# Kernel optimization log

Hardware: AMD Instinct MI355X
Metric: run time of the kernel (lower is better)

## Reference

```python
import jax, jax.numpy as jnp
import numpy as np
import math

B, L, DIM = 128, 192, 512
NTOKEN = 100
MAX_BONDS = 6
MAX_LEN = 192


def _sinusoidal_pe(max_len, dim):
    pos = np.arange(max_len, dtype=np.float32)[:, None]
    div = np.exp(np.arange(0, dim, 2, dtype=np.float32) * (-math.log(10000.0) / dim))
    pe = np.zeros((max_len, dim), dtype=np.float32)
    pe[:, 0::2] = np.sin(pos * div)
    pe[:, 1::2] = np.cos(pos * div)
    return jnp.asarray(pe[:, None, :])  # [max_len, 1, dim]


def setup_inputs() -> dict:
    key = jax.random.key(0)
    ks = jax.random.split(key, 16)
    s = 0.02
    inp = {
        "element": jax.random.randint(ks[0], (B, L), 0, NTOKEN),
        "bond": jax.random.randint(ks[1], (B, L, MAX_BONDS), 0, L),
        "aroma": jax.random.randint(ks[2], (B, L), 0, 2),
        "charge": jax.random.randint(ks[3], (B, L), 0, 6),
        "segment": jax.random.randint(ks[4], (B, L), 0, 30),
        # parameters
        "pe": _sinusoidal_pe(MAX_LEN, DIM),
        "E_elem": jax.random.normal(ks[5], (NTOKEN, DIM), jnp.float32) * s,
        "E_charge": jax.random.normal(ks[6], (13, DIM), jnp.float32) * s,
        "E_aroma": jax.random.normal(ks[7], (2, DIM), jnp.float32) * s,
        "E_seg": jax.random.normal(ks[8], (30, DIM), jnp.float32) * s,
        "W1": jax.random.normal(ks[9], (DIM, 4 * DIM), jnp.float32) * s,
        "b1": jnp.zeros((4 * DIM,), jnp.float32),
        "W2": jax.random.normal(ks[10], (4 * DIM, DIM), jnp.float32) * s,
        "b2": jnp.zeros((DIM,), jnp.float32),
        "W3": jax.random.normal(ks[11], (DIM, 4 * DIM), jnp.float32) * s,
        "b3": jnp.zeros((4 * DIM,), jnp.float32),
        "W4": jax.random.normal(ks[12], (4 * DIM, DIM), jnp.float32) * s,
        "b4": jnp.zeros((DIM,), jnp.float32),
        "W5": jax.random.normal(ks[13], (DIM, DIM), jnp.float32) * s,
        "b5": jnp.zeros((DIM,), jnp.float32),
    }
    return inp


def _mlp(x, W1, b1, W2, b2, W3, b3, W4, b4, W5, b5):
    x = x + jnp.maximum(x @ W1 + b1, 0.0) @ W2 + b2
    x = x + jnp.maximum(x @ W3 + b3, 0.0) @ W4 + b4
    return x @ W5 + b5


def reference(element, bond, aroma, charge, segment, pe,
              E_elem, E_charge, E_aroma, E_seg,
              W1, b1, W2, b2, W3, b3, W4, b4, W5, b5):
    b, l = element.shape
    # embeddings: all [l, b, dim]
    emb = E_elem[element.T]
    emb = emb + pe[:l]                      # [l,1,dim] broadcast (eval: dropout off)
    emb = emb + E_aroma[aroma.T]
    emb = emb + E_charge[charge.T + 6]
    emb = emb + E_seg[segment.T]
    message = _mlp(emb, W1, b1, W2, b2, W3, b3, W4, b4, W5, b5)  # [l,b,dim]
    # bond aggregation: agg[k] = sum_m message[bond[b,k,m]] excluding self-bonds
    # (equivalent to the dense one-hot einsum with the diagonal masked out)
    msg_bld = jnp.transpose(message, (1, 0, 2))          # [b,l,dim]
    g = msg_bld[jnp.arange(b)[:, None, None], bond]      # [b,l,MAX_BONDS,dim]
    mask = (bond != jnp.arange(l)[None, :, None]).astype(message.dtype)
    agg = jnp.einsum('bkmd,bkm->bkd', g, mask)           # [b,l,dim]
    return emb + jnp.transpose(agg, (1, 0, 2))           # [l,b,dim]
```

## Files before the change

### kernel.cpp

```cpp
#include <hip/hip_runtime.h>
#include <cstdint>
#include <cstddef>

typedef unsigned short u16;
typedef unsigned int u32;

typedef unsigned short u16x8 __attribute__((ext_vector_type(8)));
typedef __bf16 bf16x8 __attribute__((ext_vector_type(8)));
typedef float f32x4 __attribute__((ext_vector_type(4)));
typedef float f32x8 __attribute__((ext_vector_type(8)));

#define NB   128
#define NL   192
#define NTOK (NB * NL)
#define DIM  512
#define HID  2048

static __device__ __forceinline__ float bf2f(u16 h) {
    union { u32 u; float f; } v; v.u = ((u32)h) << 16; return v.f;
}
static __device__ __forceinline__ u16 f2bf(float f) {
    union { float f; u32 u; } v; v.f = f;
    u32 u = v.u + 0x7FFF + ((v.u >> 16) & 1);
    return (u16)(u >> 16);
}

__global__ void transpose_f2b(const float* __restrict__ in, u16* __restrict__ out,
                              int K, int N) {
    __shared__ float tile[32][33];
    int tx = threadIdx.x & 31, ty = threadIdx.x >> 5;
    int n0 = blockIdx.x * 32, k0 = blockIdx.y * 32;
#pragma unroll
    for (int i = 0; i < 4; i++)
        tile[ty + i * 8][tx] = in[(size_t)(k0 + ty + i * 8) * N + n0 + tx];
    __syncthreads();
#pragma unroll
    for (int i = 0; i < 4; i++)
        out[(size_t)(n0 + ty + i * 8) * K + k0 + tx] = f2bf(tile[tx][ty + i * 8]);
}

static __device__ __forceinline__ void add8f(float* acc, const float* p) {
    f32x8 v = *(const f32x8*)p;
#pragma unroll
    for (int i = 0; i < 8; i++) acc[i] += v[i];
}

__global__ void embed_kernel(const int* __restrict__ element, const int* __restrict__ aroma,
                             const int* __restrict__ charge, const int* __restrict__ segment,
                             const float* __restrict__ pe, const float* __restrict__ E_elem,
                             const float* __restrict__ E_charge, const float* __restrict__ E_aroma,
                             const float* __restrict__ E_seg,
                             float* __restrict__ emb32, u16* __restrict__ emb16) {
    int t = blockIdx.x * 4 + (threadIdx.x >> 6);
    int lane = threadIdx.x & 63;
    int l = t >> 7, b = t & 127;
    int d = lane * 8;
    int idx = b * NL + l;
    int e = element[idx];
    int a = aroma[idx];
    int c = charge[idx] + 6;
    int s = segment[idx];
    float acc[8] = {0, 0, 0, 0, 0, 0, 0, 0};
    add8f(acc, E_elem  + (size_t)e * DIM + d);
    add8f(acc, pe      + (size_t)l * DIM + d);
    add8f(acc, E_aroma + (size_t)a * DIM + d);
    add8f(acc, E_charge+ (size_t)c * DIM + d);
    add8f(acc, E_seg   + (size_t)s * DIM + d);
    f32x8 o32; u16x8 o16;
#pragma unroll
    for (int i = 0; i < 8; i++) { o32[i] = acc[i]; o16[i] = f2bf(acc[i]); }
    *(f32x8*)(emb32 + (size_t)t * DIM + d) = o32;
    *(u16x8*)(emb16 + (size_t)t * DIM + d) = o16;
}

__global__ __launch_bounds__(256, 2) void gemm_bt(
    const u16* __restrict__ A, const u16* __restrict__ BT,
    const float* __restrict__ bias, const u16* __restrict__ resid16,
    const float* __restrict__ resid32,
    u16* __restrict__ C, int M, int N, int K, int do_relu) {
    __shared__ __align__(16) u16 smem[3 * 128 * 32 + 3 * 256 * 32];
    u16* As = smem;
    u16* Bs = smem + 3 * 128 * 32;

    const int tid  = threadIdx.x;
    const int wave = tid >> 6;
    const int lane = tid & 63;

    const int nwg = gridDim.x;
    const int bid = blockIdx.x;
    const int wg  = ((nwg & 7) == 0) ? ((bid & 7) * (nwg >> 3) + (bid >> 3)) : bid;
    const int nt  = N >> 8;
    const int m0  = (wg / nt) * 128;
    const int n0  = (wg % nt) * 256;

    const int wm = (wave >> 1) * 64;
    const int wn = (wave & 1) * 128;
    const int lr = lane >> 2;
    const int lc = (((lane & 3) ^ ((lr >> 1) & 3)) * 8);
    const int fr = lane & 15;
    const int fq = lane >> 4;
    const int fc = ((fq ^ ((fr >> 1) & 3)) * 8);

    f32x4 acc[4][8] = {};

    const u16* Ag0 = A  + (size_t)(m0 + wave * 16 + lr) * K + lc;
    const u16* Ag1 = Ag0 + (size_t)64 * K;
    const u16* Bg0 = BT + (size_t)(n0 + wave * 16 + lr) * K + lc;
    const u16* Bg1 = Bg0 + (size_t)64 * K;
    const u16* Bg2 = Bg0 + (size_t)128 * K;
    const u16* Bg3 = Bg0 + (size_t)192 * K;
    const int sA0 = (wave * 16) * 32;
    const int sA1 = (64 + wave * 16) * 32;
    const int sB0 = (wave * 16) * 32;
    const int sB1 = (64 + wave * 16) * 32;
    const int sB2 = (128 + wave * 16) * 32;
    const int sB3 = (192 + wave * 16) * 32;

#define GLL(gp, lp) __builtin_amdgcn_global_load_lds(                            \
        (const __attribute__((address_space(1))) void*)(gp),                     \
        (__attribute__((address_space(3))) void*)(lp), 16, 0, 0)
#define STAGE(buf, k0) do {                                                      \
    GLL(Ag0 + (k0), &As[(buf) * 4096 + sA0]);                                    \
    GLL(Ag1 + (k0), &As[(buf) * 4096 + sA1]);                                    \
    GLL(Bg0 + (k0), &Bs[(buf) * 8192 + sB0]);                                    \
    GLL(Bg1 + (k0), &Bs[(buf) * 8192 + sB1]);                                    \
    GLL(Bg2 + (k0), &Bs[(buf) * 8192 + sB2]);                                    \
    GLL(Bg3 + (k0), &Bs[(buf) * 8192 + sB3]);                                    \
} while (0)

    const int kIters = K >> 5;
    STAGE(0, 0);
    STAGE(1, 32);
    STAGE(2, 64);

    int cur = 0;
    for (int k = 0; k < kIters; ++k) {
        if (k + 2 < kIters)
            asm volatile("s_waitcnt vmcnt(12)\n\ts_barrier" ::: "memory");
        else if (k + 2 == kIters)
            asm volatile("s_waitcnt vmcnt(6)\n\ts_barrier" ::: "memory");
        else
            asm volatile("s_waitcnt vmcnt(0)\n\ts_barrier" ::: "memory");

        const u16* Ab = &As[cur * 4096];
        const u16* Bb = &Bs[cur * 8192];
        bf16x8 af[4], bg[8];
#pragma unroll
        for (int i = 0; i < 4; i++)
            af[i] = *(const bf16x8*)(&Ab[(wm + i * 16 + fr) * 32 + fc]);
#pragma unroll
        for (int j = 0; j < 8; j++)
            bg[j] = *(const bf16x8*)(&Bb[(wn + j * 16 + fr) * 32 + fc]);

        __builtin_amdgcn_s_setprio(1);
#pragma unroll
        for (int i = 0; i < 4; i++)
#pragma unroll
            for (int j = 0; j < 8; j++)
                acc[i][j] = __builtin_amdgcn_mfma_f32_16x16x32_bf16(
                    af[i], bg[j], acc[i][j], 0, 0, 0);
        __builtin_amdgcn_s_setprio(0);

        if (k + 3 < kIters) {
            asm volatile("s_barrier" ::: "memory");
            STAGE(cur, (k + 3) << 5);
        }
        cur = (cur == 2) ? 0 : cur + 1;
    }
#undef STAGE
#undef GLL

    __syncthreads();
#define CSTR 264
#pragma unroll
    for (int j = 0; j < 8; j++) {
        int n = n0 + wn + j * 16 + fr;
        float bv = bias[n];
#pragma unroll
        for (int i = 0; i < 4; i++) {
#pragma unroll
            for (int r = 0; r < 4; r++) {
                int m = m0 + wm + i * 16 + fq * 4 + r;
                float v = acc[i][j][r] + bv;
                if (do_relu) v = fmaxf(v, 0.0f);
                if (resid16) v += bf2f(resid16[(size_t)m * N + n]);
                if (resid32) v += resid32[(size_t)m * N + n];
                smem[(wm + i * 16 + fq * 4 + r) * CSTR + wn + j * 16 + fr] = f2bf(v);
            }
        }
    }
    __syncthreads();
    {
        const int erow = tid >> 5;
        const int ecol = (tid & 31) * 8;
#pragma unroll
        for (int rr = 0; rr < 16; ++rr) {
            int row = rr * 8 + erow;
            *(u16x8*)(C + (size_t)(m0 + row) * N + n0 + ecol) =
                *(const u16x8*)(&smem[row * CSTR + ecol]);
        }
    }
#undef CSTR
}

__global__ void agg_kernel(const float* __restrict__ emb32, const u16* __restrict__ msg,
                           const int* __restrict__ bond, float* __restrict__ out) {
    int t = blockIdx.x * 4 + (threadIdx.x >> 6);
    int lane = threadIdx.x & 63;
    int l = t >> 7, b = t & 127;
    int d = lane * 8;
    float acc[8];
    {
        f32x8 v = *(const f32x8*)(emb32 + (size_t)t * DIM + d);
#pragma unroll
        for (int i = 0; i < 8; i++) acc[i] = v[i];
    }
    const int* bp = bond + ((size_t)b * NL + l) * 6;
#pragma unroll
    for (int m = 0; m < 6; m++) {
        int j = bp[m];
        if (j != l) {
            u16x8 g = *(const u16x8*)(msg + ((size_t)j * NB + b) * DIM + d);
#pragma unroll
            for (int i = 0; i < 8; i++) acc[i] += bf2f(g[i]);
        }
    }
    f32x8 o;
#pragma unroll
    for (int i = 0; i < 8; i++) o[i] = acc[i];
    *(f32x8*)(out + (size_t)t * DIM + d) = o;
}

extern "C" void kernel_launch(void* const* d_in, const int* in_sizes, int n_in,
                              void* d_out, int out_size, void* d_ws, size_t ws_size,
                              hipStream_t stream) {
    const int* element = (const int*)d_in[0];
    const int* bond    = (const int*)d_in[1];
    const int* aroma   = (const int*)d_in[2];
    const int* charge  = (const int*)d_in[3];
    const int* segment = (const int*)d_in[4];
    const float* pe      = (const float*)d_in[5];
    const float* E_elem  = (const float*)d_in[6];
    const float* E_charge= (const float*)d_in[7];
    const float* E_aroma = (const float*)d_in[8];
    const float* E_seg   = (const float*)d_in[9];
    const float* W1 = (const float*)d_in[10];
    const float* b1 = (const float*)d_in[11];
    const float* W2 = (const float*)d_in[12];
    const float* b2 = (const float*)d_in[13];
    const float* W3 = (const float*)d_in[14];
    const float* b3 = (const float*)d_in[15];
    const float* W4 = (const float*)d_in[16];
    const float* b4 = (const float*)d_in[17];
    const float* W5 = (const float*)d_in[18];
    const float* b5 = (const float*)d_in[19];

    float* emb32 = (float*)d_out;

    char* ws = (char*)d_ws;
    size_t woff = 0;
    auto take = [&](size_t bytes) -> u16* {
        u16* p = (u16*)(ws + woff);
        woff += (bytes + 255) & ~(size_t)255;
        return p;
    };
    u16* W1T = take((size_t)HID * DIM * 2);
    u16* W2T = take((size_t)DIM * HID * 2);
    u16* W3T = take((size_t)HID * DIM * 2);
    u16* W4T = take((size_t)DIM * HID * 2);
    u16* W5T = take((size_t)DIM * DIM * 2);
    u16* emb16 = take((size_t)NTOK * DIM * 2);
    u16* msg   = take((size_t)NTOK * DIM * 2);

    static const int ncs[] = {1, 2, 3, 4, 6, 8, 12, 16, 24, 32, 48, 64, 96, 192};
    int CM = 128;
    for (int nc : ncs) {
        int cm = NTOK / nc;
        size_t need = woff + ((size_t)cm * HID * 2 + 256)
                           + ((size_t)cm * DIM * 2 + 256) * 2;
        if (need <= ws_size) { CM = cm; break; }
    }
    u16* hC  = take((size_t)CM * HID * 2);
    u16* xaC = take((size_t)CM * DIM * 2);
    u16* xbC = take((size_t)CM * DIM * 2);

    transpose_f2b<<<dim3(HID / 32, DIM / 32), 256, 0, stream>>>(W1, W1T, DIM, HID);
    transpose_f2b<<<dim3(DIM / 32, HID / 32), 256, 0, stream>>>(W2, W2T, HID, DIM);
    transpose_f2b<<<dim3(HID / 32, DIM / 32), 256, 0, stream>>>(W3, W3T, DIM, HID);
    transpose_f2b<<<dim3(DIM / 32, HID / 32), 256, 0, stream>>>(W4, W4T, HID, DIM);
    transpose_f2b<<<dim3(DIM / 32, DIM / 32), 256, 0, stream>>>(W5, W5T, DIM, DIM);

    embed_kernel<<<NTOK / 4, 256, 0, stream>>>(element, aroma, charge, segment, pe,
                                               E_elem, E_charge, E_aroma, E_seg,
                                               emb32, emb16);

    for (int c0 = 0; c0 < NTOK; c0 += CM) {
        const u16* x16 = emb16 + (size_t)c0 * DIM;
        const float* x32 = emb32 + (size_t)c0 * DIM;
        u16* msgC = msg + (size_t)c0 * DIM;
        int mt = CM / 128;
        gemm_bt<<<dim3(mt * (HID / 256)), 256, 0, stream>>>(x16, W1T, b1, nullptr, nullptr, hC,  CM, HID, DIM, 1);
        gemm_bt<<<dim3(mt * (DIM / 256)), 256, 0, stream>>>(hC,  W2T, b2, nullptr, x32,     xaC, CM, DIM, HID, 0);
        gemm_bt<<<dim3(mt * (HID / 256)), 256, 0, stream>>>(xaC, W3T, b3, nullptr, nullptr, hC,  CM, HID, DIM, 1);
        gemm_bt<<<dim3(mt * (DIM / 256)), 256, 0, stream>>>(hC,  W4T, b4, xaC,    nullptr,  xbC, CM, DIM, HID, 0);
        gemm_bt<<<dim3(mt * (DIM / 256)), 256, 0, stream>>>(xbC, W5T, b5, nullptr, nullptr, msgC, CM, DIM, DIM, 0);
    }

    agg_kernel<<<NTOK / 4, 256, 0, stream>>>(emb32, msg, bond, (float*)d_out);
}
```

Before: 517.4 us.

## Enlarge GEMM tile to 256x256 with 8 waves and 4-stage split A/B pipeline

The GEMM now uses 512-thread workgroups, each computing a 256x256 output tile, doubling reuse of each B tile per block. The K loop uses a 4-deep LDS ring where A and B prefetches are issued separately, interleaved with two half-iteration MFMA groups and an intra-iteration barrier. Fewer, larger blocks reduce global traffic per FLOP. In exchange, per-block LDS rises to about 132KB and the grid is halved, which may limit occupancy or leave CUs idle when the chunk is small.

```diff
diff --git a/kernel.cpp b/kernel.cpp
--- a/kernel.cpp
+++ b/kernel.cpp
@@ -73,14 +73,12 @@
     *(u16x8*)(emb16 + (size_t)t * DIM + d) = o16;
 }
 
-__global__ __launch_bounds__(256, 2) void gemm_bt(
+__global__ __launch_bounds__(512, 2) void gemm_bt(
     const u16* __restrict__ A, const u16* __restrict__ BT,
     const float* __restrict__ bias, const u16* __restrict__ resid16,
     const float* __restrict__ resid32,
     u16* __restrict__ C, int M, int N, int K, int do_relu) {
-    __shared__ __align__(16) u16 smem[3 * 128 * 32 + 3 * 256 * 32];
-    u16* As = smem;
-    u16* Bs = smem + 3 * 128 * 32;
+    __shared__ __align__(16) u16 smem[256 * 264];
 
     const int tid  = threadIdx.x;
     const int wave = tid >> 6;
@@ -90,102 +88,108 @@
     const int bid = blockIdx.x;
     const int wg  = ((nwg & 7) == 0) ? ((bid & 7) * (nwg >> 3) + (bid >> 3)) : bid;
     const int nt  = N >> 8;
-    const int m0  = (wg / nt) * 128;
+    const int m0  = (wg / nt) * 256;
     const int n0  = (wg % nt) * 256;
 
-    const int wm = (wave >> 1) * 64;
-    const int wn = (wave & 1) * 128;
-    const int lr = lane >> 2;
-    const int lc = (((lane & 3) ^ ((lr >> 1) & 3)) * 8);
-    const int fr = lane & 15;
-    const int fq = lane >> 4;
-    const int fc = ((fq ^ ((fr >> 1) & 3)) * 8);
-
-    f32x4 acc[4][8] = {};
+    const int wmh = wave >> 2;
+    const int wnq = wave & 3;
+    const int lr  = lane >> 2;
+    const int lc  = (((lane & 3) ^ ((lr >> 1) & 3)) * 8);
+    const int fr  = lane & 15;
+    const int fq  = lane >> 4;
+    const int fc  = ((fq ^ ((fr >> 1) & 3)) * 8);
+
+    f32x4 acc[8][4] = {};
 
     const u16* Ag0 = A  + (size_t)(m0 + wave * 16 + lr) * K + lc;
-    const u16* Ag1 = Ag0 + (size_t)64 * K;
+    const u16* Ag1 = Ag0 + (size_t)128 * K;
     const u16* Bg0 = BT + (size_t)(n0 + wave * 16 + lr) * K + lc;
-    const u16* Bg1 = Bg0 + (size_t)64 * K;
-    const u16* Bg2 = Bg0 + (size_t)128 * K;
-    const u16* Bg3 = Bg0 + (size_t)192 * K;
-    const int sA0 = (wave * 16) * 32;
-    const int sA1 = (64 + wave * 16) * 32;
-    const int sB0 = (wave * 16) * 32;
-    const int sB1 = (64 + wave * 16) * 32;
-    const int sB2 = (128 + wave * 16) * 32;
-    const int sB3 = (192 + wave * 16) * 32;
+    const u16* Bg1 = Bg0 + (size_t)128 * K;
+    const int sR0 = (wave * 16) * 32;
+    const int sR1 = (128 + wave * 16) * 32;
 
 #define GLL(gp, lp) __builtin_amdgcn_global_load_lds(                            \
         (const __attribute__((address_space(1))) void*)(gp),                     \
         (__attribute__((address_space(3))) void*)(lp), 16, 0, 0)
-#define STAGE(buf, k0) do {                                                      \
-    GLL(Ag0 + (k0), &As[(buf) * 4096 + sA0]);                                    \
-    GLL(Ag1 + (k0), &As[(buf) * 4096 + sA1]);                                    \
-    GLL(Bg0 + (k0), &Bs[(buf) * 8192 + sB0]);                                    \
-    GLL(Bg1 + (k0), &Bs[(buf) * 8192 + sB1]);                                    \
-    GLL(Bg2 + (k0), &Bs[(buf) * 8192 + sB2]);                                    \
-    GLL(Bg3 + (k0), &Bs[(buf) * 8192 + sB3]);                                    \
+#define STAGE_A(buf, kt) do {                                                    \
+    GLL(Ag0 + (size_t)(kt) * 32, &smem[(buf) * 8192 + sR0]);                     \
+    GLL(Ag1 + (size_t)(kt) * 32, &smem[(buf) * 8192 + sR1]);                     \
 } while (0)
-
-    const int kIters = K >> 5;
-    STAGE(0, 0);
-    STAGE(1, 32);
-    STAGE(2, 64);
-
-    int cur = 0;
-    for (int k = 0; k < kIters; ++k) {
-        if (k + 2 < kIters)
-            asm volatile("s_waitcnt vmcnt(12)\n\ts_barrier" ::: "memory");
-        else if (k + 2 == kIters)
-            asm volatile("s_waitcnt vmcnt(6)\n\ts_barrier" ::: "memory");
+#define STAGE_B(buf, kt) do {                                                    \
+    GLL(Bg0 + (size_t)(kt) * 32, &smem[32768 + (buf) * 8192 + sR0]);             \
+    GLL(Bg1 + (size_t)(kt) * 32, &smem[32768 + (buf) * 8192 + sR1]);             \
+} while (0)
+
+    const int nk = K >> 5;
+    STAGE_A(0, 0); STAGE_B(0, 0);
+    STAGE_A(1, 1); STAGE_B(1, 1);
+    STAGE_A(2, 2); STAGE_B(2, 2);
+
+    for (int t = 0; t < nk; ++t) {
+        if (t + 2 < nk)
+            asm volatile("s_waitcnt vmcnt(8)\n\ts_barrier" ::: "memory");
+        else if (t + 1 < nk)
+            asm volatile("s_waitcnt vmcnt(4)\n\ts_barrier" ::: "memory");
         else
             asm volatile("s_waitcnt vmcnt(0)\n\ts_barrier" ::: "memory");
 
-        const u16* Ab = &As[cur * 4096];
-        const u16* Bb = &Bs[cur * 8192];
-        bf16x8 af[4], bg[8];
+        const u16* Ab = &smem[(t & 3) * 8192];
+        const u16* Bb = &smem[32768 + (t & 3) * 8192];
+
+        bf16x8 af[4], bg[4];
 #pragma unroll
         for (int i = 0; i < 4; i++)
-            af[i] = *(const bf16x8*)(&Ab[(wm + i * 16 + fr) * 32 + fc]);
-#pragma unroll
-        for (int j = 0; j < 8; j++)
-            bg[j] = *(const bf16x8*)(&Bb[(wn + j * 16 + fr) * 32 + fc]);
+            af[i] = *(const bf16x8*)(&Ab[(wmh * 128 + i * 16 + fr) * 32 + fc]);
+#pragma unroll
+        for (int j = 0; j < 4; j++)
+            bg[j] = *(const bf16x8*)(&Bb[(wnq * 64 + j * 16 + fr) * 32 + fc]);
+        if (t + 3 < nk) STAGE_A((t + 3) & 3, t + 3);
 
         __builtin_amdgcn_s_setprio(1);
 #pragma unroll
         for (int i = 0; i < 4; i++)
 #pragma unroll
-            for (int j = 0; j < 8; j++)
+            for (int j = 0; j < 4; j++)
                 acc[i][j] = __builtin_amdgcn_mfma_f32_16x16x32_bf16(
                     af[i], bg[j], acc[i][j], 0, 0, 0);
         __builtin_amdgcn_s_setprio(0);
 
-        if (k + 3 < kIters) {
-            asm volatile("s_barrier" ::: "memory");
-            STAGE(cur, (k + 3) << 5);
-        }
-        cur = (cur == 2) ? 0 : cur + 1;
-    }
-#undef STAGE
+        asm volatile("s_barrier" ::: "memory");
+
+#pragma unroll
+        for (int i = 0; i < 4; i++)
+            af[i] = *(const bf16x8*)(&Ab[(wmh * 128 + (i + 4) * 16 + fr) * 32 + fc]);
+        if (t + 3 < nk) STAGE_B((t + 3) & 3, t + 3);
+
+        __builtin_amdgcn_s_setprio(1);
+#pragma unroll
+        for (int i = 0; i < 4; i++)
+#pragma unroll
+            for (int j = 0; j < 4; j++)
+                acc[i + 4][j] = __builtin_amdgcn_mfma_f32_16x16x32_bf16(
+                    af[i], bg[j], acc[i + 4][j], 0, 0, 0);
+        __builtin_amdgcn_s_setprio(0);
+    }
+#undef STAGE_A
+#undef STAGE_B
 #undef GLL
 
     __syncthreads();
 #define CSTR 264
 #pragma unroll
-    for (int j = 0; j < 8; j++) {
-        int n = n0 + wn + j * 16 + fr;
+    for (int j = 0; j < 4; j++) {
+        int n = n0 + wnq * 64 + j * 16 + fr;
         float bv = bias[n];
 #pragma unroll
-        for (int i = 0; i < 4; i++) {
+        for (int i = 0; i < 8; i++) {
 #pragma unroll
             for (int r = 0; r < 4; r++) {
-                int m = m0 + wm + i * 16 + fq * 4 + r;
+                int m = m0 + wmh * 128 + i * 16 + fq * 4 + r;
                 float v = acc[i][j][r] + bv;
                 if (do_relu) v = fmaxf(v, 0.0f);
                 if (resid16) v += bf2f(resid16[(size_t)m * N + n]);
                 if (resid32) v += resid32[(size_t)m * N + n];
-                smem[(wm + i * 16 + fq * 4 + r) * CSTR + wn + j * 16 + fr] = f2bf(v);
+                smem[(wmh * 128 + i * 16 + fq * 4 + r) * CSTR + wnq * 64 + j * 16 + fr] = f2bf(v);
             }
         }
     }
@@ -195,7 +199,7 @@
         const int ecol = (tid & 31) * 8;
 #pragma unroll
         for (int rr = 0; rr < 16; ++rr) {
-            int row = rr * 8 + erow;
+            int row = rr * 16 + erow;
             *(u16x8*)(C + (size_t)(m0 + row) * N + n0 + ecol) =
                 *(const u16x8*)(&smem[row * CSTR + ecol]);
         }
@@ -272,10 +276,11 @@
     u16* emb16 = take((size_t)NTOK * DIM * 2);
     u16* msg   = take((size_t)NTOK * DIM * 2);
 
-    static const int ncs[] = {1, 2, 3, 4, 6, 8, 12, 16, 24, 32, 48, 64, 96, 192};
-    int CM = 128;
+    static const int ncs[] = {1, 2, 3, 4, 6, 8, 12, 16, 24, 32, 48, 96};
+    int CM = 256;
     for (int nc : ncs) {
         int cm = NTOK / nc;
+        if (cm % 256 != 0) continue;
         size_t need = woff + ((size_t)cm * HID * 2 + 256)
                            + ((size_t)cm * DIM * 2 + 256) * 2;
         if (need <= ws_size) { CM = cm; break; }
@@ -298,12 +303,12 @@
         const u16* x16 = emb16 + (size_t)c0 * DIM;
         const float* x32 = emb32 + (size_t)c0 * DIM;
         u16* msgC = msg + (size_t)c0 * DIM;
-        int mt = CM / 128;
-        gemm_bt<<<dim3(mt * (HID / 256)), 256, 0, stream>>>(x16, W1T, b1, nullptr, nullptr, hC,  CM, HID, DIM, 1);
-        gemm_bt<<<dim3(mt * (DIM / 256)), 256, 0, stream>>>(hC,  W2T, b2, nullptr, x32,     xaC, CM, DIM, HID, 0);
-        gemm_bt<<<dim3(mt * (HID / 256)), 256, 0, stream>>>(xaC, W3T, b3, nullptr, nullptr, hC,  CM, HID, DIM, 1);
-        gemm_bt<<<dim3(mt * (DIM / 256)), 256, 0, stream>>>(hC,  W4T, b4, xaC,    nullptr,  xbC, CM, DIM, HID, 0);
-        gemm_bt<<<dim3(mt * (DIM / 256)), 256, 0, stream>>>(xbC, W5T, b5, nullptr, nullptr, msgC, CM, DIM, DIM, 0);
+        int mt = CM / 256;
+        gemm_bt<<<dim3(mt * (HID / 256)), 512, 0, stream>>>(x16, W1T, b1, nullptr, nullptr, hC,  CM, HID, DIM, 1);
+        gemm_bt<<<dim3(mt * (DIM / 256)), 512, 0, stream>>>(hC,  W2T, b2, nullptr, x32,     xaC, CM, DIM, HID, 0);
+        gemm_bt<<<dim3(mt * (HID / 256)), 512, 0, stream>>>(xaC, W3T, b3, nullptr, nullptr, hC,  CM, HID, DIM, 1);
+        gemm_bt<<<dim3(mt * (DIM / 256)), 512, 0, stream>>>(hC,  W4T, b4, xaC,    nullptr,  xbC, CM, DIM, HID, 0);
+        gemm_bt<<<dim3(mt * (DIM / 256)), 512, 0, stream>>>(xbC, W5T, b5, nullptr, nullptr, msgC, CM, DIM, DIM, 0);
     }
 
     agg_kernel<<<NTOK / 4, 256, 0, stream>>>(emb32, msg, bond, (float*)d_out);
```

Result: faster. 505.7 us (-2.3%).
